# Kernel tuning notes

Measured on AMD Instinct MI355X. Metric: run time of the kernel, lower is better.

The kernel has to match this reference:

```python
import jax, jax.numpy as jnp
import numpy as np

EPS = 1e-08

def setup_inputs() -> dict:
    key = jax.random.key(0)
    kH, kF, kQ, kK, kV = jax.random.split(key, 5)
    B, N, d = 8192, 16, 512
    H = jax.random.normal(kH, (B, N, d), dtype=jnp.float32)
    F_raw = jax.random.uniform(kF, (B, N), dtype=jnp.float32)
    F = F_raw / jnp.sum(F_raw, axis=-1, keepdims=True)  # fractions sum to 1
    s = 1.0 / np.sqrt(d)
    W_Q = jax.random.normal(kQ, (d, d), dtype=jnp.float32) * s
    W_K = jax.random.normal(kK, (d, d), dtype=jnp.float32) * s
    W_V = jax.random.normal(kV, (d, d), dtype=jnp.float32) * s
    return {"H": H, "F": F, "W_Q": W_Q, "W_K": W_K, "W_V": W_V}

def reference(H, F, W_Q, W_K, W_V):
    d = H.shape[-1]
    scale = jnp.asarray(d, H.dtype) ** 0.5
    # nn.Linear(d, d, bias=False): y = x @ W.T
    Q = jnp.einsum('bnd,ed->bne', H, W_Q)
    K = jnp.einsum('bnd,ed->bne', H, W_K)
    V = jnp.einsum('bnd,ed->bne', H, W_V)
    scores = jnp.einsum('bqd,bkd->bqk', Q, K) / scale  # [B,N,N]
    scores = scores + jnp.log(F + EPS)[:, None, :]      # fraction bias over keys
    alpha = jax.nn.softmax(scores, axis=-1)
    h_attn = jnp.einsum('bqk,bkd->bqd', alpha, V)
    h_out = H + h_attn                                  # residual
    h_poly = jnp.einsum('bn,bnd->bd', F, h_out)         # fraction-weighted pool
    return h_poly
```

## Files before the change

kernel.cpp:

```cpp
#include <hip/hip_runtime.h>

typedef __bf16 bf16x8 __attribute__((ext_vector_type(8)));
typedef float f32x4 __attribute__((ext_vector_type(4)));

__device__ __forceinline__ unsigned short f2bf(float f) {
    unsigned int u = __builtin_bit_cast(unsigned int, f);
    u += 0x7fffu + ((u >> 16) & 1u);
    return (unsigned short)(u >> 16);
}
__device__ __forceinline__ float bf2f(unsigned short u) {
    return __builtin_bit_cast(float, (unsigned)u << 16);
}

__device__ __forceinline__ unsigned swz1k(unsigned byte) {
    return byte ^ ((byte >> 6) & 0x70u);
}

__device__ __forceinline__ void bar_lgkm() {
    asm volatile("s_waitcnt lgkmcnt(0)\n\ts_barrier" ::: "memory");
}

__global__ __launch_bounds__(256) void prep_kernel(
    const float* __restrict__ Wq, const float* __restrict__ Wk,
    const float* __restrict__ Wv, unsigned short* __restrict__ Pc,
    unsigned short* __restrict__ Wvb)
{
    int b = blockIdx.x;
    if (b < 1024) {
        int j0 = (b >> 4) * 8;
        int kc = b & 15;
        int jloc = threadIdx.x >> 5;
        int t = threadIdx.x & 31;
        int j = j0 + jloc, d = kc * 32 + t;
        float acc = 0.f;
        #pragma unroll 8
        for (int e = 0; e < 512; ++e)
            acc = fmaf(Wk[e * 512 + j], Wq[e * 512 + d], acc);
        Pc[((kc * 512) + j) * 32 + t] = f2bf(acc);
    } else {
        int i = (b - 1024) * 256 + (int)threadIdx.x;
        Wvb[i] = f2bf(Wv[i]);
    }
}

__device__ __forceinline__ void issue_q(int q, int tid, const float4* hsrc, float4 (&hq)[2]) {
    #pragma unroll
    for (int r = 0; r < 2; ++r) {
        int flat = r * 1024 + tid;
        hq[r] = hsrc[(flat >> 5) * 128 + q * 32 + (flat & 31)];
    }
}

__device__ __forceinline__ void convert_q(int q, int tid, char* HBF, float4 (&hq)[2]) {
    #pragma unroll
    for (int r = 0; r < 2; ++r) {
        int flat = r * 1024 + tid;
        int row = flat >> 5, ch = flat & 31;
        ushort4 bv;
        bv.x = f2bf(hq[r].x); bv.y = f2bf(hq[r].y);
        bv.z = f2bf(hq[r].z); bv.w = f2bf(hq[r].w);
        *(ushort4*)(HBF + swz1k((unsigned)row * 1024u + (unsigned)(q * 32 + ch) * 8u)) = bv;
    }
}

template<bool PREF>
__device__ __forceinline__ void gemm_q(
    int kcbase, int tid, int rl, int kg,
    const unsigned short* bptr, char* HBF,
    bf16x8 (&st0)[2], bf16x8 (&st1)[2],
    f32x4 (&acc)[4][2],
    float4 (&hq)[2], const float4* hsrc, int hq_q)
{
    #pragma unroll
    for (int k = 0; k < 4; ++k) {
        const int kc = kcbase + k;
        bf16x8 bn[2];
        if (kc + 2 < 16) {
            #pragma unroll
            for (int jj = 0; jj < 2; ++jj)
                bn[jj] = *(const bf16x8*)(bptr + (kc + 2) * 16384 + jj * 512);
        }
        if (PREF && k == 1) {
            __builtin_amdgcn_sched_barrier(0);
            issue_q(hq_q, tid, hsrc, hq);
            __builtin_amdgcn_sched_barrier(0);
        }
        bf16x8 a[4];
        #pragma unroll
        for (int i = 0; i < 4; ++i) {
            unsigned off = (unsigned)(i * 16 + rl) * 1024u + (unsigned)kc * 64u + (unsigned)kg * 16u;
            a[i] = *(bf16x8*)(HBF + swz1k(off));
        }
        #pragma unroll
        for (int i = 0; i < 4; ++i)
            #pragma unroll
            for (int jj = 0; jj < 2; ++jj)
                acc[i][jj] = __builtin_amdgcn_mfma_f32_16x16x32_bf16(a[i], st0[jj], acc[i][jj], 0, 0, 0);
        #pragma unroll
        for (int jj = 0; jj < 2; ++jj) { st0[jj] = st1[jj]; st1[jj] = bn[jj]; }
    }
}

__global__ __launch_bounds__(1024, 4) void attn_main_kernel(
    const float* __restrict__ H, const float* __restrict__ F,
    const unsigned short* __restrict__ Pc,
    float* __restrict__ out, unsigned short* __restrict__ g_ws)
{
    extern __shared__ char smem[];
    char* HBF  = smem;
    char* TBF  = smem + 65536;
    float* wbuf = (float*)(smem + 131072);
    float* FL   = (float*)(smem + 131328);
    float* LFL  = (float*)(smem + 131584);

    const int tid = threadIdx.x;
    const int wv = tid >> 6;
    const int ln = tid & 63;
    const int rl = ln & 15;
    const int kg = ln >> 4;
    const int blk = blockIdx.x;
    const long long gr0 = (long long)blk * 64;
    const float4* hsrc = (const float4*)(H + gr0 * 512);

    float fval = 0.f;
    if (tid < 64) fval = F[blk * 64 + tid];

    float4 hqA[2], hqB[2];
    issue_q(0, tid, hsrc, hqA);

    const unsigned short* bptr = Pc + ((wv * 32 + rl) * 32 + kg * 8);
    bf16x8 st0[2], st1[2];
    #pragma unroll
    for (int jj = 0; jj < 2; ++jj) st0[jj] = *(const bf16x8*)(bptr + 0 * 16384 + jj * 512);
    #pragma unroll
    for (int jj = 0; jj < 2; ++jj) st1[jj] = *(const bf16x8*)(bptr + 1 * 16384 + jj * 512);

    issue_q(1, tid, hsrc, hqB);

    if (tid < 64) {
        FL[tid] = fval;
        LFL[tid] = logf(fval + 1e-8f);
    }

    f32x4 acc[4][2];
    #pragma unroll
    for (int i = 0; i < 4; ++i)
        #pragma unroll
        for (int jj = 0; jj < 2; ++jj)
            acc[i][jj] = f32x4{0.f, 0.f, 0.f, 0.f};

    convert_q(0, tid, HBF, hqA);
    bar_lgkm();
    gemm_q<true >(0,  tid, rl, kg, bptr, HBF, st0, st1, acc, hqA, hsrc, 2);
    convert_q(1, tid, HBF, hqB);
    bar_lgkm();
    gemm_q<true >(4,  tid, rl, kg, bptr, HBF, st0, st1, acc, hqB, hsrc, 3);
    convert_q(2, tid, HBF, hqA);
    bar_lgkm();
    gemm_q<false>(8,  tid, rl, kg, bptr, HBF, st0, st1, acc, hqA, hsrc, 0);
    convert_q(3, tid, HBF, hqB);
    bar_lgkm();
    gemm_q<false>(12, tid, rl, kg, bptr, HBF, st0, st1, acc, hqB, hsrc, 0);

    #pragma unroll
    for (int i = 0; i < 4; ++i)
        #pragma unroll
        for (int jj = 0; jj < 2; ++jj)
            #pragma unroll
            for (int p = 0; p < 4; ++p) {
                unsigned row = (unsigned)(i * 16 + kg * 4 + p);
                unsigned col = (unsigned)(wv * 32 + jj * 16 + rl);
                *(unsigned short*)(TBF + swz1k(row * 1024u + col * 2u)) = f2bf(acc[i][jj][p]);
            }
    bar_lgkm();

    if (wv < 4) {
        f32x4 sc0 = f32x4{0.f,0.f,0.f,0.f}, sc1 = sc0, sc2 = sc0, sc3 = sc0;
        __builtin_amdgcn_s_setprio(1);
        #pragma unroll
        for (int kc = 0; kc < 16; ++kc) {
            unsigned off = (unsigned)(wv * 16 + rl) * 1024u + (unsigned)kc * 64u + (unsigned)kg * 16u;
            bf16x8 aT = *(bf16x8*)(TBF + swz1k(off));
            bf16x8 bH = *(bf16x8*)(HBF + swz1k(off));
            if ((kc & 3) == 0) sc0 = __builtin_amdgcn_mfma_f32_16x16x32_bf16(aT, bH, sc0, 0, 0, 0);
            else if ((kc & 3) == 1) sc1 = __builtin_amdgcn_mfma_f32_16x16x32_bf16(aT, bH, sc1, 0, 0, 0);
            else if ((kc & 3) == 2) sc2 = __builtin_amdgcn_mfma_f32_16x16x32_bf16(aT, bH, sc2, 0, 0, 0);
            else sc3 = __builtin_amdgcn_mfma_f32_16x16x32_bf16(aT, bH, sc3, 0, 0, 0);
        }
        __builtin_amdgcn_s_setprio(0);
        f32x4 sc;
        #pragma unroll
        for (int p = 0; p < 4; ++p) sc[p] = (sc0[p] + sc1[p]) + (sc2[p] + sc3[p]);

        float bias = LFL[wv * 16 + rl];
        float alpha[4];
        #pragma unroll
        for (int p = 0; p < 4; ++p) {
            float s = sc[p] * 0.044194173824159216f + bias;
            float m = s;
            m = fmaxf(m, __shfl_xor(m, 8));
            m = fmaxf(m, __shfl_xor(m, 4));
            m = fmaxf(m, __shfl_xor(m, 2));
            m = fmaxf(m, __shfl_xor(m, 1));
            float e = expf(s - m);
            float sum = e;
            sum += __shfl_xor(sum, 8);
            sum += __shfl_xor(sum, 4);
            sum += __shfl_xor(sum, 2);
            sum += __shfl_xor(sum, 1);
            alpha[p] = e / sum;
        }
        float part = 0.f;
        #pragma unroll
        for (int p = 0; p < 4; ++p) part += FL[wv * 16 + kg * 4 + p] * alpha[p];
        part += __shfl_xor(part, 16);
        part += __shfl_xor(part, 32);
        if (ln < 16) wbuf[wv * 16 + ln] = part;
    } else if (wv < 12) {
        int u = wv - 4;
        int bb = u >> 1, dh = u & 1;
        const long long Bg = (long long)blk * 4 + bb;
        int d0 = dh * 256 + ln * 4;
        float o[4];
        #pragma unroll
        for (int q = 0; q < 4; ++q) o[q] = 0.f;
        #pragma unroll
        for (int k = 0; k < 16; ++k) {
            unsigned off = (unsigned)(bb * 16 + k) * 1024u + (unsigned)d0 * 2u;
            ushort4 h = *(ushort4*)(HBF + swz1k(off));
            float fk = FL[bb * 16 + k];
            o[0] = fmaf(fk, bf2f(h.x), o[0]); o[1] = fmaf(fk, bf2f(h.y), o[1]);
            o[2] = fmaf(fk, bf2f(h.z), o[2]); o[3] = fmaf(fk, bf2f(h.w), o[3]);
        }
        float4 oa; oa.x = o[0]; oa.y = o[1]; oa.z = o[2]; oa.w = o[3];
        *(float4*)(out + Bg * 512 + d0) = oa;
    }
    bar_lgkm();

    {
        int bb = wv >> 2, q4 = wv & 3;
        const long long Bg = (long long)blk * 4 + bb;
        int d0 = q4 * 128 + ln * 2;
        float g0 = 0.f, g1 = 0.f;
        #pragma unroll
        for (int k = 0; k < 16; ++k) {
            unsigned off = (unsigned)(bb * 16 + k) * 1024u + (unsigned)d0 * 2u;
            ushort2 h = *(ushort2*)(HBF + swz1k(off));
            float wk = wbuf[bb * 16 + k];
            g0 = fmaf(wk, bf2f(h.x), g0); g1 = fmaf(wk, bf2f(h.y), g1);
        }
        ushort2 g2; g2.x = f2bf(g0); g2.y = f2bf(g1);
        *(ushort2*)(g_ws + Bg * 512 + d0) = g2;
    }
}

__global__ __launch_bounds__(256) void out_gemm_kernel(
    const unsigned short* __restrict__ g_ws,
    const unsigned short* __restrict__ Wvb,
    float* __restrict__ out)
{
    extern __shared__ char smem[];
    const int tid = threadIdx.x;
    const int wv = tid >> 6, ln = tid & 63;
    const int rl = ln & 15, kg = ln >> 4;
    const long long r0 = (long long)blockIdx.x * 32;
    {
        const uint4* src = (const uint4*)(g_ws + r0 * 512);
        #pragma unroll
        for (int q = 0; q < 8; ++q) {
            int idx = q * 256 + tid;
            *(uint4*)(smem + swz1k((unsigned)idx * 16u)) = src[idx];
        }
    }
    __syncthreads();
    f32x4 acc[2][8];
    #pragma unroll
    for (int i = 0; i < 2; ++i)
        #pragma unroll
        for (int jj = 0; jj < 8; ++jj)
            acc[i][jj] = f32x4{0.f, 0.f, 0.f, 0.f};
    for (int kc = 0; kc < 16; ++kc) {
        bf16x8 a[2];
        #pragma unroll
        for (int i = 0; i < 2; ++i) {
            unsigned off = (unsigned)(i * 16 + rl) * 1024u + (unsigned)kc * 64u + (unsigned)kg * 16u;
            a[i] = *(bf16x8*)(smem + swz1k(off));
        }
        bf16x8 bfr[8];
        #pragma unroll
        for (int jj = 0; jj < 8; ++jj) {
            int n = wv * 128 + jj * 16 + rl;
            bfr[jj] = *(const bf16x8*)(Wvb + n * 512 + kc * 32 + kg * 8);
        }
        #pragma unroll
        for (int i = 0; i < 2; ++i)
            #pragma unroll
            for (int jj = 0; jj < 8; ++jj)
                acc[i][jj] = __builtin_amdgcn_mfma_f32_16x16x32_bf16(a[i], bfr[jj], acc[i][jj], 0, 0, 0);
    }
    #pragma unroll
    for (int i = 0; i < 2; ++i)
        #pragma unroll
        for (int jj = 0; jj < 8; ++jj)
            #pragma unroll
            for (int p = 0; p < 4; ++p) {
                int row = i * 16 + kg * 4 + p;
                int col = wv * 128 + jj * 16 + rl;
                out[(r0 + row) * 512 + col] += acc[i][jj][p];
            }
}

extern "C" void kernel_launch(void* const* d_in, const int* in_sizes, int n_in,
                              void* d_out, int out_size, void* d_ws, size_t ws_size,
                              hipStream_t stream)
{
    const float* H  = (const float*)d_in[0];
    const float* F  = (const float*)d_in[1];
    const float* Wq = (const float*)d_in[2];
    const float* Wk = (const float*)d_in[3];
    const float* Wv = (const float*)d_in[4];
    float* out = (float*)d_out;

    unsigned short* Pc  = (unsigned short*)d_ws;
    unsigned short* Wvb = Pc + 262144;
    unsigned short* g   = Wvb + 262144;
    (void)in_sizes; (void)n_in; (void)out_size; (void)ws_size;

    prep_kernel<<<dim3(2048), dim3(256), 0, stream>>>(Wq, Wk, Wv, Pc, Wvb);
    attn_main_kernel<<<dim3(2048), dim3(1024), 131840, stream>>>(H, F, Pc, out, g);
    out_gemm_kernel<<<dim3(256), dim3(256), 32768, stream>>>(g, Wvb, out);
}
```

Before: 196.3 us.

## Split score MFMA and softmax across all 16 waves with LDS partial sums

The score computation, previously done by 4 waves each running 16 serial MFMAs, is split so every wave computes a quarter of the K-reduction and writes partial scores to a padded LDS slab. All 1024 threads then sum the partials and run softmax one element per lane, and a final fused pass computes both the F-weighted residual output and the attention-weighted pooling in one sweep over H. This aims to remove the idle-wave imbalance in the attention phase. In exchange it adds an extra barrier and raises LDS use from about 129 KB to about 147 KB per block.

```diff
diff --git a/kernel.cpp b/kernel.cpp
--- a/kernel.cpp
+++ b/kernel.cpp
@@ -19,6 +19,7 @@
 __device__ __forceinline__ void bar_lgkm() {
     asm volatile("s_waitcnt lgkmcnt(0)\n\ts_barrier" ::: "memory");
 }
+#define SB() __builtin_amdgcn_sched_barrier(0)
 
 __global__ __launch_bounds__(256) void prep_kernel(
     const float* __restrict__ Wq, const float* __restrict__ Wk,
@@ -81,9 +82,9 @@
                 bn[jj] = *(const bf16x8*)(bptr + (kc + 2) * 16384 + jj * 512);
         }
         if (PREF && k == 1) {
-            __builtin_amdgcn_sched_barrier(0);
+            SB();
             issue_q(hq_q, tid, hsrc, hq);
-            __builtin_amdgcn_sched_barrier(0);
+            SB();
         }
         bf16x8 a[4];
         #pragma unroll
@@ -109,9 +110,10 @@
     extern __shared__ char smem[];
     char* HBF  = smem;
     char* TBF  = smem + 65536;
-    float* wbuf = (float*)(smem + 131072);
-    float* FL   = (float*)(smem + 131328);
-    float* LFL  = (float*)(smem + 131584);
+    float* PS  = (float*)(smem + 131072);
+    float* WP  = (float*)(smem + 148480);
+    float* FL  = (float*)(smem + 149504);
+    float* LFL = (float*)(smem + 149760);
 
     const int tid = threadIdx.x;
     const int wv = tid >> 6;
@@ -174,81 +176,67 @@
             }
     bar_lgkm();
 
-    if (wv < 4) {
-        f32x4 sc0 = f32x4{0.f,0.f,0.f,0.f}, sc1 = sc0, sc2 = sc0, sc3 = sc0;
-        __builtin_amdgcn_s_setprio(1);
-        #pragma unroll
-        for (int kc = 0; kc < 16; ++kc) {
-            unsigned off = (unsigned)(wv * 16 + rl) * 1024u + (unsigned)kc * 64u + (unsigned)kg * 16u;
+    {
+        const int b = wv >> 2, kcg = wv & 3;
+        f32x4 sc = f32x4{0.f, 0.f, 0.f, 0.f};
+        #pragma unroll
+        for (int i = 0; i < 4; ++i) {
+            const int kc = kcg * 4 + i;
+            unsigned off = (unsigned)(b * 16 + rl) * 1024u + (unsigned)kc * 64u + (unsigned)kg * 16u;
             bf16x8 aT = *(bf16x8*)(TBF + swz1k(off));
             bf16x8 bH = *(bf16x8*)(HBF + swz1k(off));
-            if ((kc & 3) == 0) sc0 = __builtin_amdgcn_mfma_f32_16x16x32_bf16(aT, bH, sc0, 0, 0, 0);
-            else if ((kc & 3) == 1) sc1 = __builtin_amdgcn_mfma_f32_16x16x32_bf16(aT, bH, sc1, 0, 0, 0);
-            else if ((kc & 3) == 2) sc2 = __builtin_amdgcn_mfma_f32_16x16x32_bf16(aT, bH, sc2, 0, 0, 0);
-            else sc3 = __builtin_amdgcn_mfma_f32_16x16x32_bf16(aT, bH, sc3, 0, 0, 0);
-        }
-        __builtin_amdgcn_s_setprio(0);
-        f32x4 sc;
-        #pragma unroll
-        for (int p = 0; p < 4; ++p) sc[p] = (sc0[p] + sc1[p]) + (sc2[p] + sc3[p]);
-
-        float bias = LFL[wv * 16 + rl];
-        float alpha[4];
-        #pragma unroll
-        for (int p = 0; p < 4; ++p) {
-            float s = sc[p] * 0.044194173824159216f + bias;
-            float m = s;
-            m = fmaxf(m, __shfl_xor(m, 8));
-            m = fmaxf(m, __shfl_xor(m, 4));
-            m = fmaxf(m, __shfl_xor(m, 2));
-            m = fmaxf(m, __shfl_xor(m, 1));
-            float e = expf(s - m);
-            float sum = e;
-            sum += __shfl_xor(sum, 8);
-            sum += __shfl_xor(sum, 4);
-            sum += __shfl_xor(sum, 2);
-            sum += __shfl_xor(sum, 1);
-            alpha[p] = e / sum;
-        }
-        float part = 0.f;
-        #pragma unroll
-        for (int p = 0; p < 4; ++p) part += FL[wv * 16 + kg * 4 + p] * alpha[p];
+            sc = __builtin_amdgcn_mfma_f32_16x16x32_bf16(aT, bH, sc, 0, 0, 0);
+        }
+        float* slab = PS + wv * 272;
+        #pragma unroll
+        for (int p = 0; p < 4; ++p)
+            slab[(kg * 4 + p) * 17 + rl] = sc[p];
+    }
+    bar_lgkm();
+
+    {
+        const int b = tid >> 8, q = (tid >> 4) & 15, k = tid & 15;
+        float s = 0.f;
+        #pragma unroll
+        for (int g = 0; g < 4; ++g)
+            s += PS[(b * 4 + g) * 272 + q * 17 + k];
+        s = s * 0.044194173824159216f + LFL[b * 16 + k];
+        float m = s;
+        m = fmaxf(m, __shfl_xor(m, 8));
+        m = fmaxf(m, __shfl_xor(m, 4));
+        m = fmaxf(m, __shfl_xor(m, 2));
+        m = fmaxf(m, __shfl_xor(m, 1));
+        float e = expf(s - m);
+        float sum = e;
+        sum += __shfl_xor(sum, 8);
+        sum += __shfl_xor(sum, 4);
+        sum += __shfl_xor(sum, 2);
+        sum += __shfl_xor(sum, 1);
+        float part = FL[b * 16 + q] * (e / sum);
         part += __shfl_xor(part, 16);
         part += __shfl_xor(part, 32);
-        if (ln < 16) wbuf[wv * 16 + ln] = part;
-    } else if (wv < 12) {
-        int u = wv - 4;
-        int bb = u >> 1, dh = u & 1;
-        const long long Bg = (long long)blk * 4 + bb;
-        int d0 = dh * 256 + ln * 4;
-        float o[4];
-        #pragma unroll
-        for (int q = 0; q < 4; ++q) o[q] = 0.f;
+        if (ln < 16) WP[(b * 4 + (wv & 3)) * 16 + ln] = part;
+    }
+    bar_lgkm();
+
+    {
+        const int b = wv >> 2, dq = wv & 3;
+        const long long Bg = (long long)blk * 4 + b;
+        const int d0 = dq * 128 + ln * 2;
+        float o0 = 0.f, o1 = 0.f, g0 = 0.f, g1 = 0.f;
         #pragma unroll
         for (int k = 0; k < 16; ++k) {
-            unsigned off = (unsigned)(bb * 16 + k) * 1024u + (unsigned)d0 * 2u;
-            ushort4 h = *(ushort4*)(HBF + swz1k(off));
-            float fk = FL[bb * 16 + k];
-            o[0] = fmaf(fk, bf2f(h.x), o[0]); o[1] = fmaf(fk, bf2f(h.y), o[1]);
-            o[2] = fmaf(fk, bf2f(h.z), o[2]); o[3] = fmaf(fk, bf2f(h.w), o[3]);
-        }
-        float4 oa; oa.x = o[0]; oa.y = o[1]; oa.z = o[2]; oa.w = o[3];
-        *(float4*)(out + Bg * 512 + d0) = oa;
-    }
-    bar_lgkm();
-
-    {
-        int bb = wv >> 2, q4 = wv & 3;
-        const long long Bg = (long long)blk * 4 + bb;
-        int d0 = q4 * 128 + ln * 2;
-        float g0 = 0.f, g1 = 0.f;
-        #pragma unroll
-        for (int k = 0; k < 16; ++k) {
-            unsigned off = (unsigned)(bb * 16 + k) * 1024u + (unsigned)d0 * 2u;
+            unsigned off = (unsigned)(b * 16 + k) * 1024u + (unsigned)d0 * 2u;
             ushort2 h = *(ushort2*)(HBF + swz1k(off));
-            float wk = wbuf[bb * 16 + k];
-            g0 = fmaf(wk, bf2f(h.x), g0); g1 = fmaf(wk, bf2f(h.y), g1);
-        }
+            float h0 = bf2f(h.x), h1 = bf2f(h.y);
+            float fk = FL[b * 16 + k];
+            float wk = WP[(b * 4 + 0) * 16 + k] + WP[(b * 4 + 1) * 16 + k]
+                     + WP[(b * 4 + 2) * 16 + k] + WP[(b * 4 + 3) * 16 + k];
+            o0 = fmaf(fk, h0, o0); o1 = fmaf(fk, h1, o1);
+            g0 = fmaf(wk, h0, g0); g1 = fmaf(wk, h1, g1);
+        }
+        float2 o2; o2.x = o0; o2.y = o1;
+        *(float2*)(out + Bg * 512 + d0) = o2;
         ushort2 g2; g2.x = f2bf(g0); g2.y = f2bf(g1);
         *(ushort2*)(g_ws + Bg * 512 + d0) = g2;
     }
@@ -327,6 +315,6 @@
     (void)in_sizes; (void)n_in; (void)out_size; (void)ws_size;
 
     prep_kernel<<<dim3(2048), dim3(256), 0, stream>>>(Wq, Wk, Wv, Pc, Wvb);
-    attn_main_kernel<<<dim3(2048), dim3(1024), 131840, stream>>>(H, F, Pc, out, g);
+    attn_main_kernel<<<dim3(2048), dim3(1024), 150016, stream>>>(H, F, Pc, out, g);
     out_gemm_kernel<<<dim3(256), dim3(256), 32768, stream>>>(g, Wvb, out);
 }
```

New measurement: 203.3 us. 1.04x slower.

## Issue all H quarter loads upfront, deepen B prefetch, use packed bf16 convert

Applied to the files above, without the earlier changes.

All four quarters of the H tile are now loaded into registers at kernel start instead of being prefetched mid-GEMM. The weight-fragment prefetch ring grows from two stages to three. The f32-to-bf16 conversion uses the hardware v_cvt_pk_bf16_f32 instruction instead of software rounding. The goal is more memory-level parallelism and fewer ALU ops, at the cost of higher register pressure under 1024-thread blocks with launch_bounds(1024,4), which could cause spills.

```diff
diff --git a/kernel.cpp b/kernel.cpp
--- a/kernel.cpp
+++ b/kernel.cpp
@@ -11,6 +11,11 @@
 __device__ __forceinline__ float bf2f(unsigned short u) {
     return __builtin_bit_cast(float, (unsigned)u << 16);
 }
+__device__ __forceinline__ unsigned cvtpk(float lo, float hi) {
+    unsigned r;
+    asm("v_cvt_pk_bf16_f32 %0, %1, %2" : "=v"(r) : "v"(lo), "v"(hi));
+    return r;
+}
 
 __device__ __forceinline__ unsigned swz1k(unsigned byte) {
     return byte ^ ((byte >> 6) & 0x70u);
@@ -19,6 +24,7 @@
 __device__ __forceinline__ void bar_lgkm() {
     asm volatile("s_waitcnt lgkmcnt(0)\n\ts_barrier" ::: "memory");
 }
+#define SB() __builtin_amdgcn_sched_barrier(0)
 
 __global__ __launch_bounds__(256) void prep_kernel(
     const float* __restrict__ Wq, const float* __restrict__ Wk,
@@ -56,34 +62,27 @@
     for (int r = 0; r < 2; ++r) {
         int flat = r * 1024 + tid;
         int row = flat >> 5, ch = flat & 31;
-        ushort4 bv;
-        bv.x = f2bf(hq[r].x); bv.y = f2bf(hq[r].y);
-        bv.z = f2bf(hq[r].z); bv.w = f2bf(hq[r].w);
-        *(ushort4*)(HBF + swz1k((unsigned)row * 1024u + (unsigned)(q * 32 + ch) * 8u)) = bv;
-    }
-}
-
-template<bool PREF>
+        uint2 bv;
+        bv.x = cvtpk(hq[r].x, hq[r].y);
+        bv.y = cvtpk(hq[r].z, hq[r].w);
+        *(uint2*)(HBF + swz1k((unsigned)row * 1024u + (unsigned)(q * 32 + ch) * 8u)) = bv;
+    }
+}
+
 __device__ __forceinline__ void gemm_q(
-    int kcbase, int tid, int rl, int kg,
+    int kcbase, int rl, int kg,
     const unsigned short* bptr, char* HBF,
-    bf16x8 (&st0)[2], bf16x8 (&st1)[2],
-    f32x4 (&acc)[4][2],
-    float4 (&hq)[2], const float4* hsrc, int hq_q)
+    bf16x8 (&st0)[2], bf16x8 (&st1)[2], bf16x8 (&st2)[2],
+    f32x4 (&acc)[4][2])
 {
     #pragma unroll
     for (int k = 0; k < 4; ++k) {
         const int kc = kcbase + k;
         bf16x8 bn[2];
-        if (kc + 2 < 16) {
+        if (kc + 3 < 16) {
             #pragma unroll
             for (int jj = 0; jj < 2; ++jj)
-                bn[jj] = *(const bf16x8*)(bptr + (kc + 2) * 16384 + jj * 512);
-        }
-        if (PREF && k == 1) {
-            __builtin_amdgcn_sched_barrier(0);
-            issue_q(hq_q, tid, hsrc, hq);
-            __builtin_amdgcn_sched_barrier(0);
+                bn[jj] = *(const bf16x8*)(bptr + (kc + 3) * 16384 + jj * 512);
         }
         bf16x8 a[4];
         #pragma unroll
@@ -97,7 +96,7 @@
             for (int jj = 0; jj < 2; ++jj)
                 acc[i][jj] = __builtin_amdgcn_mfma_f32_16x16x32_bf16(a[i], st0[jj], acc[i][jj], 0, 0, 0);
         #pragma unroll
-        for (int jj = 0; jj < 2; ++jj) { st0[jj] = st1[jj]; st1[jj] = bn[jj]; }
+        for (int jj = 0; jj < 2; ++jj) { st0[jj] = st1[jj]; st1[jj] = st2[jj]; st2[jj] = bn[jj]; }
     }
 }
 
@@ -125,17 +124,23 @@
     float fval = 0.f;
     if (tid < 64) fval = F[blk * 64 + tid];
 
-    float4 hqA[2], hqB[2];
+    const unsigned short* bptr = Pc + ((wv * 32 + rl) * 32 + kg * 8);
+
+    float4 hqA[2], hqB[2], hqC[2], hqD[2];
     issue_q(0, tid, hsrc, hqA);
-
-    const unsigned short* bptr = Pc + ((wv * 32 + rl) * 32 + kg * 8);
-    bf16x8 st0[2], st1[2];
+    SB();
+    bf16x8 st0[2], st1[2], st2[2];
     #pragma unroll
     for (int jj = 0; jj < 2; ++jj) st0[jj] = *(const bf16x8*)(bptr + 0 * 16384 + jj * 512);
     #pragma unroll
     for (int jj = 0; jj < 2; ++jj) st1[jj] = *(const bf16x8*)(bptr + 1 * 16384 + jj * 512);
-
+    #pragma unroll
+    for (int jj = 0; jj < 2; ++jj) st2[jj] = *(const bf16x8*)(bptr + 2 * 16384 + jj * 512);
+    SB();
     issue_q(1, tid, hsrc, hqB);
+    issue_q(2, tid, hsrc, hqC);
+    issue_q(3, tid, hsrc, hqD);
+    SB();
 
     if (tid < 64) {
         FL[tid] = fval;
@@ -151,16 +156,16 @@
 
     convert_q(0, tid, HBF, hqA);
     bar_lgkm();
-    gemm_q<true >(0,  tid, rl, kg, bptr, HBF, st0, st1, acc, hqA, hsrc, 2);
+    gemm_q(0,  rl, kg, bptr, HBF, st0, st1, st2, acc);
     convert_q(1, tid, HBF, hqB);
     bar_lgkm();
-    gemm_q<true >(4,  tid, rl, kg, bptr, HBF, st0, st1, acc, hqB, hsrc, 3);
-    convert_q(2, tid, HBF, hqA);
-    bar_lgkm();
-    gemm_q<false>(8,  tid, rl, kg, bptr, HBF, st0, st1, acc, hqA, hsrc, 0);
-    convert_q(3, tid, HBF, hqB);
-    bar_lgkm();
-    gemm_q<false>(12, tid, rl, kg, bptr, HBF, st0, st1, acc, hqB, hsrc, 0);
+    gemm_q(4,  rl, kg, bptr, HBF, st0, st1, st2, acc);
+    convert_q(2, tid, HBF, hqC);
+    bar_lgkm();
+    gemm_q(8,  rl, kg, bptr, HBF, st0, st1, st2, acc);
+    convert_q(3, tid, HBF, hqD);
+    bar_lgkm();
+    gemm_q(12, rl, kg, bptr, HBF, st0, st1, st2, acc);
 
     #pragma unroll
     for (int i = 0; i < 4; ++i)
```

Result: slower. 213.9 us (+9.0%).
